# Kernel tuning notes

Measured on AMD Instinct MI355X. Metric: run time of the kernel, lower is better.

## Reference

```python
import jax, jax.numpy as jnp
import numpy as np

# ---- static config (mirrors init_kwargs + fixed setup box dims) ----
PC_MIN = jnp.array([0.0, -40.0, -3.0])
VOXEL_SIZE = jnp.array([0.05, 0.05, 0.1])
STRIDE = 4                     # pool_cfg.STRIDE and multi_scale_3d_strides['x_conv4']
EXTEND = 2.0                   # model_cfg.ROI_EXTEND_FACTOR
GRID_ZYX = (10, 400, 352)      # sparse spatial shape after stride-4 downsample [z,y,x]
# grid_size = round(extended_dims / voxel_size / STRIDE) for fixed dims [6.4,3.2,1.6]
GX, GY, GZ = 64, 32, 4
G = GX * GY * GZ
N_VOX, C = 200_000, 128
M = 64
KX, KY, KZ = 7, 7, 3


def setup_inputs() -> dict:
    key = jax.random.key(0)
    k1, k2, k3, k4, k5, k6, k7, k8, k9 = jax.random.split(key, 9)
    ctr = jnp.stack([
        jax.random.uniform(k1, (M,), minval=10.0, maxval=60.0),
        jax.random.uniform(k2, (M,), minval=-25.0, maxval=25.0),
        jax.random.uniform(k3, (M,), minval=-1.5, maxval=0.5)], axis=-1)
    dims = jnp.tile(jnp.array([[6.4, 3.2, 1.6]], jnp.float32), (M, 1))  # fixed -> static grid
    yaw = jax.random.uniform(k4, (M, 1), minval=-np.pi, maxval=np.pi)
    rois = jnp.concatenate([ctr, dims, yaw], axis=-1).astype(jnp.float32)
    proto_box = jnp.array([0.0, 0.0, 0.0, 6.4, 3.2, 1.6, 0.3], jnp.float32)
    voxel_feats = jax.random.normal(k5, (N_VOX, C), jnp.float32)
    feat_proto = jax.random.normal(k6, (1, KX, KY, KZ, C), jnp.float32) * 0.1
    zc = jax.random.randint(k7, (N_VOX,), 0, GRID_ZYX[0])
    yc = jax.random.randint(k8, (N_VOX,), 0, GRID_ZYX[1])
    xc = jax.random.randint(k9, (N_VOX,), 0, GRID_ZYX[2])
    voxel_coords = jnp.stack([jnp.zeros_like(zc), zc, yc, xc], -1).astype(jnp.int32)
    return dict(rois=rois, proto_box=proto_box, voxel_feats=voxel_feats,
                feat_proto=feat_proto, voxel_coords=voxel_coords)


def _dense_grid_points(box):
    # get_dense_grid_points: row-major (x,y,z) index order, matches torch nonzero()
    idx = jnp.stack(jnp.meshgrid(jnp.arange(GX), jnp.arange(GY), jnp.arange(GZ),
                                 indexing='ij'), -1).reshape(-1, 3).astype(jnp.float32)
    gs = jnp.array([GX, GY, GZ], jnp.float32)
    return (idx + 0.5) / gs * box[3:6] - box[3:6] / 2.0  # (G,3)


def _rotate_z(pts, ang):
    # common_utils.rotate_points_along_z: pts @ [[c,s,0],[-s,c,0],[0,0,1]]
    c, s = jnp.cos(ang), jnp.sin(ang)
    R = jnp.stack([jnp.stack([c, s, 0.0 * c]),
                   jnp.stack([-s, c, 0.0 * c]),
                   jnp.stack([0.0 * c, 0.0 * c, 1.0 + 0.0 * c])])
    return pts @ R


def reference(rois, proto_box, voxel_feats, feat_proto, voxel_coords):
    # generate_voxel2pinds: dense [Z,Y,X] grid of voxel row indices, -1 = empty
    v2p = -jnp.ones(GRID_ZYX, jnp.int32)
    v2p = v2p.at[voxel_coords[:, 1], voxel_coords[:, 2], voxel_coords[:, 3]].set(
        jnp.arange(N_VOX, dtype=jnp.int32))

    def per_roi(box):
        box = box.at[3:5].multiply(EXTEND)                 # xy_dim_extend
        local = _dense_grid_points(box)                    # (G,3)
        xyz = _rotate_z(local, box[6]) + box[:3]           # global roi grid points
        coords = jnp.floor((xyz - PC_MIN) / VOXEL_SIZE)    # '//' floor-div semantics
        coords = jnp.floor(coords / STRIDE).astype(jnp.int32)
        xc, yc, zc = coords[:, 0], coords[:, 1], coords[:, 2]
        inb = ((zc >= 0) & (zc < GRID_ZYX[0]) & (yc >= 0) & (yc < GRID_ZYX[1]) &
               (xc >= 0) & (xc < GRID_ZYX[2]))
        pidx = v2p[jnp.clip(zc, 0, GRID_ZYX[0] - 1),
                   jnp.clip(yc, 0, GRID_ZYX[1] - 1),
                   jnp.clip(xc, 0, GRID_ZYX[2] - 1)]
        valid = inb & (pidx >= 0)
        feat = jnp.where(valid[:, None], voxel_feats[jnp.clip(pidx, 0)], 0.0)  # (G,C)
        return feat, xyz

    feats, grid_xyz = jax.vmap(per_roi)(rois)              # (M,G,C), (M,G,3)
    vol = feats.reshape(M, GX, GY, GZ, C).transpose(0, 4, 1, 2, 3)   # NCDHW
    kern = feat_proto.transpose(0, 4, 1, 2, 3)                        # (1,C,KX,KY,KZ)
    pads = [(KX // 2,) * 2, (KY // 2,) * 2, (KZ // 2,) * 2]           # ceil((k-1)/2)
    mm = jax.lax.conv_general_dilated(vol, kern, (1, 1, 1), pads,
                                      dimension_numbers=('NCDHW', 'OIDHW', 'NCDHW'))
    # fresh BatchNorm3d(1) applied per-ROI (batch 1 each call): per-sample norm
    mu = jnp.mean(mm, axis=(1, 2, 3, 4), keepdims=True)
    var = jnp.var(mm, axis=(1, 2, 3, 4), keepdims=True)
    mm = (mm - mu) / jnp.sqrt(var + 1e-5)
    idx = jnp.minimum(jnp.argmax(mm.reshape(M, -1), axis=1), G - 1)
    sel = jnp.take_along_axis(grid_xyz, idx[:, None, None], axis=1)[:, 0, :]  # (M,3)
    rois_new = jnp.tile(proto_box[None], (M, 1))
    rois_new = rois_new.at[:, :3].set(sel)
    return rois_new
```

## Files before the change

kernel.cpp:

```cpp
#include <hip/hip_runtime.h>
#include <stdint.h>

#define GRID_Z 10
#define GRID_Y 400
#define GRID_X 352
#define NGRID (GRID_Z * GRID_Y * GRID_X)
#define NVOX 200000
#define CCH 128
#define MROI 64
#define GXD 64
#define GYD 32
#define GZD 4
#define GCELLS 8192
#define NTAPS 147
#define FPAD 132
#define TROWS 32

__device__ __forceinline__ void cell_xyz(const float* __restrict__ roi, int g,
                                         float& X, float& Y, float& Z) {
#pragma clang fp contract(off)
    int iz = g & 3;
    int iy = (g >> 2) & 31;
    int ix = g >> 7;
    float bx = roi[3] * 2.0f;
    float by = roi[4] * 2.0f;
    float bz = roi[5];
    float lx = (ix + 0.5f) / 64.0f * bx - bx / 2.0f;
    float ly = (iy + 0.5f) / 32.0f * by - by / 2.0f;
    float lz = (iz + 0.5f) / 4.0f  * bz - bz / 2.0f;
    float c = cosf(roi[6]);
    float s = sinf(roi[6]);
    X = lx * c + ly * (-s) + roi[0];
    Y = lx * s + ly * c    + roi[1];
    Z = lz + roi[2];
}

__device__ __forceinline__ int cell_to_pidx(const float* __restrict__ roi, int g,
                                            const int* __restrict__ v2p) {
#pragma clang fp contract(off)
    float X, Y, Z;
    cell_xyz(roi, g, X, Y, Z);
    float fx = floorf((X - 0.0f)     / 0.05f);
    float fy = floorf((Y - (-40.0f)) / 0.05f);
    float fz = floorf((Z - (-3.0f))  / 0.1f);
    int cx = (int)floorf(fx / 4.0f);
    int cy = (int)floorf(fy / 4.0f);
    int cz = (int)floorf(fz / 4.0f);
    int p = -1;
    if (cz >= 0 && cz < GRID_Z && cy >= 0 && cy < GRID_Y && cx >= 0 && cx < GRID_X)
        p = v2p[(cz * GRID_Y + cy) * GRID_X + cx];
    return p;
}

__global__ void k_scatter(const int* __restrict__ vcoords, int* __restrict__ v2p,
                          int* __restrict__ cnt) {
    int i = blockIdx.x * 256 + threadIdx.x;
    if (blockIdx.x == 0 && threadIdx.x < MROI) cnt[threadIdx.x] = 0;
    if (i >= NVOX) return;
    int z = vcoords[i * 4 + 1];
    int y = vcoords[i * 4 + 2];
    int x = vcoords[i * 4 + 3];
    atomicMax(&v2p[(z * GRID_Y + y) * GRID_X + x], i);
}

__global__ void k_build(const float* __restrict__ rois, const int* __restrict__ v2p,
                        unsigned* __restrict__ list, int* __restrict__ cnt) {
    int g = blockIdx.x * 256 + threadIdx.x;
    int m = blockIdx.y;
    int lane = threadIdx.x & 63;
    int p = cell_to_pidx(rois + m * 7, g, v2p);
    bool v = p >= 0;
    unsigned long long bal = __ballot(v);
    int nset = __popcll(bal);
    int base = 0;
    if (lane == 0 && nset) base = atomicAdd(&cnt[m], nset);
    base = __shfl(base, 0, 64);
    if (v) {
        int pos = __popcll(bal & ((1ull << lane) - 1ull));
        list[m * GCELLS + base + pos] = ((unsigned)p << 13) | (unsigned)g;
    }
}

__global__ __launch_bounds__(256) void k_dots(
        const float* __restrict__ vfeat, const float* __restrict__ fproto,
        const unsigned* __restrict__ list, const int* __restrict__ cnt,
        float* __restrict__ partial) {
    __shared__ float    sscore[GCELLS];
    __shared__ float    sfeat[TROWS * FPAD];
    __shared__ unsigned sg[TROWS];

    const int m    = blockIdx.y;
    const int NSd  = gridDim.x;
    const int tid  = threadIdx.x;
    const int w    = tid >> 6;
    const int lane = tid & 63;
    const int vi   = lane & 7;
    const int ti   = (lane >> 3) & 7;
    const int n    = cnt[m];
    const unsigned* lst = list + m * GCELLS;
    const int tbase = w * 40 + ti;

    int tkx[5], tky[5], tkz[5], tok[5];
    #pragma unroll
    for (int b = 0; b < 5; ++b) {
        int t = tbase + 8 * b;
        tok[b] = t < NTAPS;
        int tc = tok[b] ? t : (NTAPS - 1);
        int kx  = tc / 21;
        int rem = tc - kx * 21;
        tkx[b] = kx; tky[b] = rem / 3; tkz[b] = rem - tky[b] * 3;
    }
    {
        float4* s4 = (float4*)sscore;
        #pragma unroll
        for (int i = 0; i < GCELLS / 4 / 256; ++i)
            s4[tid + 256 * i] = make_float4(0.f, 0.f, 0.f, 0.f);
    }
    for (int vt0 = blockIdx.x * TROWS; vt0 < n; vt0 += TROWS * NSd) {
        __syncthreads();
        {
            int r = tid >> 3, q = tid & 7, v = vt0 + r;
            unsigned e = 0xFFFFFFFFu;
            if (v < n) e = lst[v];
            if (q == 0) sg[r] = e;
            if (e != 0xFFFFFFFFu) {
                int p = (int)(e >> 13);
                const float4* src = (const float4*)(vfeat + (size_t)p * CCH) + q * 4;
                float4* drow = (float4*)(sfeat + r * FPAD + q * 16);
                #pragma unroll
                for (int j = 0; j < 4; ++j) drow[j] = src[j];
            }
        }
        __syncthreads();
        float acc[4][5];
        #pragma unroll
        for (int a = 0; a < 4; ++a)
            #pragma unroll
            for (int b = 0; b < 5; ++b) acc[a][b] = 0.0f;
        #pragma unroll 1
        for (int k = 0; k < CCH; k += 4) {
            float4 f[4];
            #pragma unroll
            for (int a = 0; a < 4; ++a)
                f[a] = *(const float4*)&sfeat[(vi + 8 * a) * FPAD + k];
            float4 wv[5];
            #pragma unroll
            for (int b = 0; b < 5; ++b)
                wv[b] = *(const float4*)(fproto + (tbase + (tok[b] ? 8 * b : 0)) * CCH + k);
            #pragma unroll
            for (int a = 0; a < 4; ++a)
                #pragma unroll
                for (int b = 0; b < 5; ++b) {
                    acc[a][b] = fmaf(f[a].x, wv[b].x, acc[a][b]);
                    acc[a][b] = fmaf(f[a].y, wv[b].y, acc[a][b]);
                    acc[a][b] = fmaf(f[a].z, wv[b].z, acc[a][b]);
                    acc[a][b] = fmaf(f[a].w, wv[b].w, acc[a][b]);
                }
        }
        #pragma unroll
        for (int b = 0; b < 5; ++b) {
            if (!tok[b]) continue;
            #pragma unroll
            for (int a = 0; a < 4; ++a) {
                unsigned e = sg[vi + 8 * a];
                if (e == 0xFFFFFFFFu) continue;
                int g  = (int)(e & 8191u);
                int cx = (g >> 7)        - (tkx[b] - 3);
                int cy = ((g >> 2) & 31) - (tky[b] - 3);
                int cz = (g & 3)         - (tkz[b] - 1);
                if ((unsigned)cx < (unsigned)GXD && (unsigned)cy < (unsigned)GYD &&
                    (unsigned)cz < (unsigned)GZD)
                    atomicAdd(&sscore[(cx << 7) | (cy << 2) | cz], acc[a][b]);
            }
        }
    }
    __syncthreads();
    {
        float* dst = partial + ((size_t)m * NSd + blockIdx.x) * GCELLS;
        const float4* s4 = (const float4*)sscore;
        float4* d4 = (float4*)dst;
        #pragma unroll
        for (int i = 0; i < GCELLS / 4 / 256; ++i)
            d4[tid + 256 * i] = s4[tid + 256 * i];
    }
}

template <int NS>
__global__ __launch_bounds__(1024) void k_argfin(
        const float* __restrict__ partial, const float* __restrict__ rois,
        const float* __restrict__ pbox, float* __restrict__ out) {
    __shared__ unsigned long long red[1024];
    int m = blockIdx.x;
    int tid = threadIdx.x;
    const float* base = partial + (size_t)m * NS * GCELLS;
    unsigned long long bk = 0ull;
    #pragma unroll
    for (int i = 0; i < GCELLS / 1024; ++i) {
        int g = tid + 1024 * i;
        float v = 0.0f;
        #pragma unroll
        for (int s = 0; s < NS; ++s) v += base[s * GCELLS + g];
        unsigned ub  = __float_as_uint(v);
        unsigned key = (ub & 0x80000000u) ? ~ub : (ub | 0x80000000u);
        unsigned long long pk =
            ((unsigned long long)key << 32) | (unsigned)(GCELLS - 1 - g);
        bk = bk > pk ? bk : pk;
    }
    red[tid] = bk;
    __syncthreads();
    for (int s = 512; s > 0; s >>= 1) {
        if (tid < s) {
            unsigned long long o = red[tid + s];
            if (o > red[tid]) red[tid] = o;
        }
        __syncthreads();
    }
    if (tid == 0) {
        int g = (GCELLS - 1) - (int)(unsigned)(red[0] & 0xFFFFFFFFu);
        float X, Y, Z;
        cell_xyz(rois + m * 7, g, X, Y, Z);
        out[m * 7 + 0] = X;
        out[m * 7 + 1] = Y;
        out[m * 7 + 2] = Z;
        out[m * 7 + 3] = pbox[3];
        out[m * 7 + 4] = pbox[4];
        out[m * 7 + 5] = pbox[5];
        out[m * 7 + 6] = pbox[6];
    }
}

extern "C" void kernel_launch(void* const* d_in, const int* in_sizes, int n_in,
                              void* d_out, int out_size, void* d_ws, size_t ws_size,
                              hipStream_t stream) {
    const float* rois    = (const float*)d_in[0];
    const float* pbox    = (const float*)d_in[1];
    const float* vfeat   = (const float*)d_in[2];
    const float* fproto  = (const float*)d_in[3];
    const int*   vcoords = (const int*)d_in[4];
    float* out = (float*)d_out;

    int*      v2p  = (int*)d_ws;
    unsigned* list = (unsigned*)(v2p + NGRID);
    int*      cnt  = (int*)(list + MROI * GCELLS);
    size_t base = ((size_t)NGRID + (size_t)MROI * GCELLS) * 4 + 256;

    int NS; float* fpartial;
    if (ws_size >= base + (size_t)12 * MROI * GCELLS * 4) {
        NS = 12; fpartial = (float*)((char*)d_ws + base);
    } else if (ws_size >= base + (size_t)8 * MROI * GCELLS * 4) {
        NS = 8;  fpartial = (float*)((char*)d_ws + base);
    } else if (ws_size >= base + (size_t)4 * MROI * GCELLS * 4) {
        NS = 4;  fpartial = (float*)((char*)d_ws + base);
    } else {
        NS = 2;  fpartial = (float*)v2p;
    }

    hipMemsetAsync(v2p, 0xFF, (size_t)NGRID * 4, stream);
    k_scatter<<<(NVOX + 255) / 256, 256, 0, stream>>>(vcoords, v2p, cnt);
    k_build  <<<dim3(GCELLS / 256, MROI), 256, 0, stream>>>(rois, v2p, list, cnt);
    k_dots   <<<dim3(NS, MROI), 256, 0, stream>>>(vfeat, fproto, list, cnt, fpartial);
    if (NS == 12)      k_argfin<12><<<MROI, 1024, 0, stream>>>(fpartial, rois, pbox, out);
    else if (NS == 8)  k_argfin<8> <<<MROI, 1024, 0, stream>>>(fpartial, rois, pbox, out);
    else if (NS == 4)  k_argfin<4> <<<MROI, 1024, 0, stream>>>(fpartial, rois, pbox, out);
    else               k_argfin<2> <<<MROI, 1024, 0, stream>>>(fpartial, rois, pbox, out);
}
```

Measured before the change: 299.1 us.

## Enlarge dot tile, atomically reduce slice scores, distribute argmax with last-block finalize

```diff
diff --git a/kernel.cpp b/kernel.cpp
--- a/kernel.cpp
+++ b/kernel.cpp
@@ -14,7 +14,8 @@
 #define GCELLS 8192
 #define NTAPS 147
 #define FPAD 132
-#define TROWS 32
+#define TROWS 64
+#define NSLC 8
 
 __device__ __forceinline__ void cell_xyz(const float* __restrict__ roi, int g,
                                          float& X, float& Y, float& Z) {
@@ -52,10 +53,8 @@
     return p;
 }
 
-__global__ void k_scatter(const int* __restrict__ vcoords, int* __restrict__ v2p,
-                          int* __restrict__ cnt) {
+__global__ void k_scatter(const int* __restrict__ vcoords, int* __restrict__ v2p) {
     int i = blockIdx.x * 256 + threadIdx.x;
-    if (blockIdx.x == 0 && threadIdx.x < MROI) cnt[threadIdx.x] = 0;
     if (i >= NVOX) return;
     int z = vcoords[i * 4 + 1];
     int y = vcoords[i * 4 + 2];
@@ -84,7 +83,7 @@
 __global__ __launch_bounds__(256) void k_dots(
         const float* __restrict__ vfeat, const float* __restrict__ fproto,
         const unsigned* __restrict__ list, const int* __restrict__ cnt,
-        float* __restrict__ partial) {
+        float* __restrict__ score) {
     __shared__ float    sscore[GCELLS];
     __shared__ float    sfeat[TROWS * FPAD];
     __shared__ unsigned sg[TROWS];
@@ -119,36 +118,36 @@
     for (int vt0 = blockIdx.x * TROWS; vt0 < n; vt0 += TROWS * NSd) {
         __syncthreads();
         {
-            int r = tid >> 3, q = tid & 7, v = vt0 + r;
+            int r = tid >> 2, q = tid & 3, v = vt0 + r;
             unsigned e = 0xFFFFFFFFu;
             if (v < n) e = lst[v];
             if (q == 0) sg[r] = e;
             if (e != 0xFFFFFFFFu) {
                 int p = (int)(e >> 13);
-                const float4* src = (const float4*)(vfeat + (size_t)p * CCH) + q * 4;
-                float4* drow = (float4*)(sfeat + r * FPAD + q * 16);
+                const float4* src = (const float4*)(vfeat + (size_t)p * CCH) + q * 8;
+                float4* drow = (float4*)(sfeat + r * FPAD + q * 32);
                 #pragma unroll
-                for (int j = 0; j < 4; ++j) drow[j] = src[j];
+                for (int j = 0; j < 8; ++j) drow[j] = src[j];
             }
         }
         __syncthreads();
-        float acc[4][5];
-        #pragma unroll
-        for (int a = 0; a < 4; ++a)
+        float acc[8][5];
+        #pragma unroll
+        for (int a = 0; a < 8; ++a)
             #pragma unroll
             for (int b = 0; b < 5; ++b) acc[a][b] = 0.0f;
         #pragma unroll 1
         for (int k = 0; k < CCH; k += 4) {
-            float4 f[4];
-            #pragma unroll
-            for (int a = 0; a < 4; ++a)
+            float4 f[8];
+            #pragma unroll
+            for (int a = 0; a < 8; ++a)
                 f[a] = *(const float4*)&sfeat[(vi + 8 * a) * FPAD + k];
             float4 wv[5];
             #pragma unroll
             for (int b = 0; b < 5; ++b)
                 wv[b] = *(const float4*)(fproto + (tbase + (tok[b] ? 8 * b : 0)) * CCH + k);
             #pragma unroll
-            for (int a = 0; a < 4; ++a)
+            for (int a = 0; a < 8; ++a)
                 #pragma unroll
                 for (int b = 0; b < 5; ++b) {
                     acc[a][b] = fmaf(f[a].x, wv[b].x, acc[a][b]);
@@ -158,16 +157,17 @@
                 }
         }
         #pragma unroll
-        for (int b = 0; b < 5; ++b) {
-            if (!tok[b]) continue;
-            #pragma unroll
-            for (int a = 0; a < 4; ++a) {
-                unsigned e = sg[vi + 8 * a];
-                if (e == 0xFFFFFFFFu) continue;
-                int g  = (int)(e & 8191u);
-                int cx = (g >> 7)        - (tkx[b] - 3);
-                int cy = ((g >> 2) & 31) - (tky[b] - 3);
-                int cz = (g & 3)         - (tkz[b] - 1);
+        for (int a = 0; a < 8; ++a) {
+            unsigned e = sg[vi + 8 * a];
+            if (e == 0xFFFFFFFFu) continue;
+            int g  = (int)(e & 8191u);
+            int gx = g >> 7, gy = (g >> 2) & 31, gz = g & 3;
+            #pragma unroll
+            for (int b = 0; b < 5; ++b) {
+                if (!tok[b]) continue;
+                int cx = gx - (tkx[b] - 3);
+                int cy = gy - (tky[b] - 3);
+                int cz = gz - (tkz[b] - 1);
                 if ((unsigned)cx < (unsigned)GXD && (unsigned)cy < (unsigned)GYD &&
                     (unsigned)cz < (unsigned)GZD)
                     atomicAdd(&sscore[(cx << 7) | (cy << 2) | cz], acc[a][b]);
@@ -175,57 +175,66 @@
         }
     }
     __syncthreads();
-    {
-        float* dst = partial + ((size_t)m * NSd + blockIdx.x) * GCELLS;
-        const float4* s4 = (const float4*)sscore;
-        float4* d4 = (float4*)dst;
-        #pragma unroll
-        for (int i = 0; i < GCELLS / 4 / 256; ++i)
-            d4[tid + 256 * i] = s4[tid + 256 * i];
-    }
-}
-
-template <int NS>
-__global__ __launch_bounds__(1024) void k_argfin(
-        const float* __restrict__ partial, const float* __restrict__ rois,
-        const float* __restrict__ pbox, float* __restrict__ out) {
-    __shared__ unsigned long long red[1024];
-    int m = blockIdx.x;
-    int tid = threadIdx.x;
-    const float* base = partial + (size_t)m * NS * GCELLS;
+    if (blockIdx.x * TROWS < n) {
+        float* dst = score + (size_t)m * GCELLS;
+        #pragma unroll
+        for (int i = 0; i < GCELLS / 256; ++i) {
+            float v = sscore[tid + 256 * i];
+            if (__float_as_uint(v) != 0u)
+                atomicAdd(&dst[tid + 256 * i], v);
+        }
+    }
+}
+
+__global__ __launch_bounds__(256) void k_amax(
+        const float* __restrict__ score, const float* __restrict__ rois,
+        const float* __restrict__ pbox, unsigned long long* __restrict__ best,
+        unsigned* __restrict__ done, float* __restrict__ out) {
+    __shared__ unsigned long long red[256];
+    __shared__ unsigned lastflag;
+    const int tid = threadIdx.x;
+    const int m = blockIdx.y;
+    const float* base = score + (size_t)m * GCELLS;
+    int c0 = blockIdx.x * (GCELLS / 8);
     unsigned long long bk = 0ull;
     #pragma unroll
-    for (int i = 0; i < GCELLS / 1024; ++i) {
-        int g = tid + 1024 * i;
-        float v = 0.0f;
-        #pragma unroll
-        for (int s = 0; s < NS; ++s) v += base[s * GCELLS + g];
+    for (int i = 0; i < GCELLS / 8 / 256; ++i) {
+        int c = c0 + tid + 256 * i;
+        float v = base[c];
         unsigned ub  = __float_as_uint(v);
         unsigned key = (ub & 0x80000000u) ? ~ub : (ub | 0x80000000u);
         unsigned long long pk =
-            ((unsigned long long)key << 32) | (unsigned)(GCELLS - 1 - g);
+            ((unsigned long long)key << 32) | (unsigned)(GCELLS - 1 - c);
         bk = bk > pk ? bk : pk;
     }
     red[tid] = bk;
     __syncthreads();
-    for (int s = 512; s > 0; s >>= 1) {
-        if (tid < s) {
-            unsigned long long o = red[tid + s];
+    for (int st = 128; st > 0; st >>= 1) {
+        if (tid < st) {
+            unsigned long long o = red[tid + st];
             if (o > red[tid]) red[tid] = o;
         }
         __syncthreads();
     }
     if (tid == 0) {
-        int g = (GCELLS - 1) - (int)(unsigned)(red[0] & 0xFFFFFFFFu);
+        atomicMax(&best[m], red[0]);
+        __threadfence();
+        unsigned d = atomicAdd(done, 1u);
+        lastflag = (d == gridDim.x * gridDim.y - 1u);
+    }
+    __syncthreads();
+    if (lastflag && tid < MROI) {
+        unsigned long long bv = atomicMax(&best[tid], 0ull);
+        int g = (GCELLS - 1) - (int)(unsigned)(bv & 0xFFFFFFFFu);
         float X, Y, Z;
-        cell_xyz(rois + m * 7, g, X, Y, Z);
-        out[m * 7 + 0] = X;
-        out[m * 7 + 1] = Y;
-        out[m * 7 + 2] = Z;
-        out[m * 7 + 3] = pbox[3];
-        out[m * 7 + 4] = pbox[4];
-        out[m * 7 + 5] = pbox[5];
-        out[m * 7 + 6] = pbox[6];
+        cell_xyz(rois + tid * 7, g, X, Y, Z);
+        out[tid * 7 + 0] = X;
+        out[tid * 7 + 1] = Y;
+        out[tid * 7 + 2] = Z;
+        out[tid * 7 + 3] = pbox[3];
+        out[tid * 7 + 4] = pbox[4];
+        out[tid * 7 + 5] = pbox[5];
+        out[tid * 7 + 6] = pbox[6];
     }
 }
 
@@ -241,26 +250,16 @@
 
     int*      v2p  = (int*)d_ws;
     unsigned* list = (unsigned*)(v2p + NGRID);
-    int*      cnt  = (int*)(list + MROI * GCELLS);
-    size_t base = ((size_t)NGRID + (size_t)MROI * GCELLS) * 4 + 256;
-
-    int NS; float* fpartial;
-    if (ws_size >= base + (size_t)12 * MROI * GCELLS * 4) {
-        NS = 12; fpartial = (float*)((char*)d_ws + base);
-    } else if (ws_size >= base + (size_t)8 * MROI * GCELLS * 4) {
-        NS = 8;  fpartial = (float*)((char*)d_ws + base);
-    } else if (ws_size >= base + (size_t)4 * MROI * GCELLS * 4) {
-        NS = 4;  fpartial = (float*)((char*)d_ws + base);
-    } else {
-        NS = 2;  fpartial = (float*)v2p;
-    }
+    float*    score = (float*)(list + (size_t)MROI * GCELLS);
+    unsigned long long* best = (unsigned long long*)(score + (size_t)MROI * GCELLS);
+    int*      cnt  = (int*)(best + MROI);
+    unsigned* done = (unsigned*)(cnt + MROI);
+    size_t zbytes = (size_t)((char*)(done + 1) - (char*)score);
 
     hipMemsetAsync(v2p, 0xFF, (size_t)NGRID * 4, stream);
-    k_scatter<<<(NVOX + 255) / 256, 256, 0, stream>>>(vcoords, v2p, cnt);
+    hipMemsetAsync(score, 0, zbytes, stream);
+    k_scatter<<<(NVOX + 255) / 256, 256, 0, stream>>>(vcoords, v2p);
     k_build  <<<dim3(GCELLS / 256, MROI), 256, 0, stream>>>(rois, v2p, list, cnt);
-    k_dots   <<<dim3(NS, MROI), 256, 0, stream>>>(vfeat, fproto, list, cnt, fpartial);
-    if (NS == 12)      k_argfin<12><<<MROI, 1024, 0, stream>>>(fpartial, rois, pbox, out);
-    else if (NS == 8)  k_argfin<8> <<<MROI, 1024, 0, stream>>>(fpartial, rois, pbox, out);
-    else if (NS == 4)  k_argfin<4> <<<MROI, 1024, 0, stream>>>(fpartial, rois, pbox, out);
-    else               k_argfin<2> <<<MROI, 1024, 0, stream>>>(fpartial, rois, pbox, out);
-}
+    k_dots   <<<dim3(NSLC, MROI), 256, 0, stream>>>(vfeat, fproto, list, cnt, score);
+    k_amax   <<<dim3(8, MROI), 256, 0, stream>>>(score, rois, pbox, best, done, out);
+}
```

New measurement: 343.3 us. 14.8% more time.

## Fuse argmax finalize into dots kernel via atomic score accumulation and last-block reduction

Applied to the files above, without the earlier changes.

```diff
diff --git a/kernel.cpp b/kernel.cpp
--- a/kernel.cpp
+++ b/kernel.cpp
@@ -15,6 +15,7 @@
 #define NTAPS 147
 #define FPAD 132
 #define TROWS 32
+#define NSLC 12
 
 __device__ __forceinline__ void cell_xyz(const float* __restrict__ roi, int g,
                                          float& X, float& Y, float& Z) {
@@ -53,9 +54,12 @@
 }
 
 __global__ void k_scatter(const int* __restrict__ vcoords, int* __restrict__ v2p,
-                          int* __restrict__ cnt) {
+                          int* __restrict__ cnt, unsigned* __restrict__ rdone) {
     int i = blockIdx.x * 256 + threadIdx.x;
-    if (blockIdx.x == 0 && threadIdx.x < MROI) cnt[threadIdx.x] = 0;
+    if (blockIdx.x == 0 && threadIdx.x < MROI) {
+        cnt[threadIdx.x] = 0;
+        rdone[threadIdx.x] = 0u;
+    }
     if (i >= NVOX) return;
     int z = vcoords[i * 4 + 1];
     int y = vcoords[i * 4 + 2];
@@ -64,9 +68,11 @@
 }
 
 __global__ void k_build(const float* __restrict__ rois, const int* __restrict__ v2p,
-                        unsigned* __restrict__ list, int* __restrict__ cnt) {
+                        unsigned* __restrict__ list, int* __restrict__ cnt,
+                        float* __restrict__ score) {
     int g = blockIdx.x * 256 + threadIdx.x;
     int m = blockIdx.y;
+    score[(size_t)m * GCELLS + g] = 0.0f;
     int lane = threadIdx.x & 63;
     int p = cell_to_pidx(rois + m * 7, g, v2p);
     bool v = p >= 0;
@@ -84,10 +90,13 @@
 __global__ __launch_bounds__(256) void k_dots(
         const float* __restrict__ vfeat, const float* __restrict__ fproto,
         const unsigned* __restrict__ list, const int* __restrict__ cnt,
-        float* __restrict__ partial) {
+        float* __restrict__ score, unsigned* __restrict__ rdone,
+        const float* __restrict__ rois, const float* __restrict__ pbox,
+        float* __restrict__ out) {
     __shared__ float    sscore[GCELLS];
     __shared__ float    sfeat[TROWS * FPAD];
     __shared__ unsigned sg[TROWS];
+    __shared__ unsigned lastflag;
 
     const int m    = blockIdx.y;
     const int NSd  = gridDim.x;
@@ -116,6 +125,7 @@
         for (int i = 0; i < GCELLS / 4 / 256; ++i)
             s4[tid + 256 * i] = make_float4(0.f, 0.f, 0.f, 0.f);
     }
+    const bool contrib = (blockIdx.x * TROWS < n);
     for (int vt0 = blockIdx.x * TROWS; vt0 < n; vt0 += TROWS * NSd) {
         __syncthreads();
         {
@@ -158,16 +168,17 @@
                 }
         }
         #pragma unroll
-        for (int b = 0; b < 5; ++b) {
-            if (!tok[b]) continue;
-            #pragma unroll
-            for (int a = 0; a < 4; ++a) {
-                unsigned e = sg[vi + 8 * a];
-                if (e == 0xFFFFFFFFu) continue;
-                int g  = (int)(e & 8191u);
-                int cx = (g >> 7)        - (tkx[b] - 3);
-                int cy = ((g >> 2) & 31) - (tky[b] - 3);
-                int cz = (g & 3)         - (tkz[b] - 1);
+        for (int a = 0; a < 4; ++a) {
+            unsigned e = sg[vi + 8 * a];
+            if (e == 0xFFFFFFFFu) continue;
+            int g  = (int)(e & 8191u);
+            int gx = g >> 7, gy = (g >> 2) & 31, gz = g & 3;
+            #pragma unroll
+            for (int b = 0; b < 5; ++b) {
+                if (!tok[b]) continue;
+                int cx = gx - (tkx[b] - 3);
+                int cy = gy - (tky[b] - 3);
+                int cz = gz - (tkz[b] - 1);
                 if ((unsigned)cx < (unsigned)GXD && (unsigned)cy < (unsigned)GYD &&
                     (unsigned)cz < (unsigned)GZD)
                     atomicAdd(&sscore[(cx << 7) | (cy << 2) | cz], acc[a][b]);
@@ -175,42 +186,40 @@
         }
     }
     __syncthreads();
-    {
-        float* dst = partial + ((size_t)m * NSd + blockIdx.x) * GCELLS;
-        const float4* s4 = (const float4*)sscore;
-        float4* d4 = (float4*)dst;
-        #pragma unroll
-        for (int i = 0; i < GCELLS / 4 / 256; ++i)
-            d4[tid + 256 * i] = s4[tid + 256 * i];
-    }
-}
-
-template <int NS>
-__global__ __launch_bounds__(1024) void k_argfin(
-        const float* __restrict__ partial, const float* __restrict__ rois,
-        const float* __restrict__ pbox, float* __restrict__ out) {
-    __shared__ unsigned long long red[1024];
-    int m = blockIdx.x;
-    int tid = threadIdx.x;
-    const float* base = partial + (size_t)m * NS * GCELLS;
+    float* dst = score + (size_t)m * GCELLS;
+    if (contrib) {
+        #pragma unroll
+        for (int i = 0; i < GCELLS / 256; ++i) {
+            float v = sscore[tid + 256 * i];
+            if (__float_as_uint(v) != 0u)
+                atomicAdd(&dst[tid + 256 * i], v);
+        }
+    }
+    __threadfence();
+    if (tid == 0) {
+        unsigned d = atomicAdd(&rdone[m], 1u);
+        lastflag = (d == (unsigned)NSd - 1u);
+    }
+    __syncthreads();
+    if (!lastflag) return;
+
     unsigned long long bk = 0ull;
     #pragma unroll
-    for (int i = 0; i < GCELLS / 1024; ++i) {
-        int g = tid + 1024 * i;
-        float v = 0.0f;
-        #pragma unroll
-        for (int s = 0; s < NS; ++s) v += base[s * GCELLS + g];
+    for (int i = 0; i < GCELLS / 256; ++i) {
+        int c = tid + 256 * i;
+        float v = atomicAdd(&dst[c], 0.0f);
         unsigned ub  = __float_as_uint(v);
         unsigned key = (ub & 0x80000000u) ? ~ub : (ub | 0x80000000u);
         unsigned long long pk =
-            ((unsigned long long)key << 32) | (unsigned)(GCELLS - 1 - g);
+            ((unsigned long long)key << 32) | (unsigned)(GCELLS - 1 - c);
         bk = bk > pk ? bk : pk;
     }
+    unsigned long long* red = reinterpret_cast<unsigned long long*>(sscore);
     red[tid] = bk;
     __syncthreads();
-    for (int s = 512; s > 0; s >>= 1) {
-        if (tid < s) {
-            unsigned long long o = red[tid + s];
+    for (int st = 128; st > 0; st >>= 1) {
+        if (tid < st) {
+            unsigned long long o = red[tid + st];
             if (o > red[tid]) red[tid] = o;
         }
         __syncthreads();
@@ -239,28 +248,15 @@
     const int*   vcoords = (const int*)d_in[4];
     float* out = (float*)d_out;
 
-    int*      v2p  = (int*)d_ws;
-    unsigned* list = (unsigned*)(v2p + NGRID);
-    int*      cnt  = (int*)(list + MROI * GCELLS);
-    size_t base = ((size_t)NGRID + (size_t)MROI * GCELLS) * 4 + 256;
-
-    int NS; float* fpartial;
-    if (ws_size >= base + (size_t)12 * MROI * GCELLS * 4) {
-        NS = 12; fpartial = (float*)((char*)d_ws + base);
-    } else if (ws_size >= base + (size_t)8 * MROI * GCELLS * 4) {
-        NS = 8;  fpartial = (float*)((char*)d_ws + base);
-    } else if (ws_size >= base + (size_t)4 * MROI * GCELLS * 4) {
-        NS = 4;  fpartial = (float*)((char*)d_ws + base);
-    } else {
-        NS = 2;  fpartial = (float*)v2p;
-    }
+    int*      v2p   = (int*)d_ws;
+    unsigned* list  = (unsigned*)(v2p + NGRID);
+    float*    score = (float*)(list + (size_t)MROI * GCELLS);
+    int*      cnt   = (int*)(score + (size_t)MROI * GCELLS);
+    unsigned* rdone = (unsigned*)(cnt + MROI);
 
     hipMemsetAsync(v2p, 0xFF, (size_t)NGRID * 4, stream);
-    k_scatter<<<(NVOX + 255) / 256, 256, 0, stream>>>(vcoords, v2p, cnt);
-    k_build  <<<dim3(GCELLS / 256, MROI), 256, 0, stream>>>(rois, v2p, list, cnt);
-    k_dots   <<<dim3(NS, MROI), 256, 0, stream>>>(vfeat, fproto, list, cnt, fpartial);
-    if (NS == 12)      k_argfin<12><<<MROI, 1024, 0, stream>>>(fpartial, rois, pbox, out);
-    else if (NS == 8)  k_argfin<8> <<<MROI, 1024, 0, stream>>>(fpartial, rois, pbox, out);
-    else if (NS == 4)  k_argfin<4> <<<MROI, 1024, 0, stream>>>(fpartial, rois, pbox, out);
-    else               k_argfin<2> <<<MROI, 1024, 0, stream>>>(fpartial, rois, pbox, out);
-}
+    k_scatter<<<(NVOX + 255) / 256, 256, 0, stream>>>(vcoords, v2p, cnt, rdone);
+    k_build  <<<dim3(GCELLS / 256, MROI), 256, 0, stream>>>(rois, v2p, list, cnt, score);
+    k_dots   <<<dim3(NSLC, MROI), 256, 0, stream>>>(vfeat, fproto, list, cnt, score,
+                                                    rdone, rois, pbox, out);
+}
```

Result: slower. 347.4 us (+16.2%).

## Compute voxel-tap dot products with split-bf16 MFMA instead of scalar FMA

Applied to the files above, without the earlier changes.

```diff
diff --git a/kernel.cpp b/kernel.cpp
--- a/kernel.cpp
+++ b/kernel.cpp
@@ -13,8 +13,22 @@
 #define GZD 4
 #define GCELLS 8192
 #define NTAPS 147
-#define FPAD 132
 #define TROWS 32
+#define NSLC 12
+#define PITCH 136
+#define NTT 10
+#define BFRAGN (NTT * 4 * 64)
+
+typedef short bf16x8 __attribute__((ext_vector_type(8)));
+typedef float f32x4 __attribute__((ext_vector_type(4)));
+
+__device__ __forceinline__ unsigned f2bf(float x) {
+    unsigned u = __float_as_uint(x);
+    return (u + 0x7FFFu + ((u >> 16) & 1u)) >> 16;
+}
+__device__ __forceinline__ float bf2f(unsigned h) {
+    return __uint_as_float(h << 16);
+}
 
 __device__ __forceinline__ void cell_xyz(const float* __restrict__ roi, int g,
                                          float& X, float& Y, float& Z) {
@@ -52,6 +66,32 @@
     return p;
 }
 
+__global__ void k_prep(const float* __restrict__ fproto,
+                       uint4* __restrict__ bH, uint4* __restrict__ bL) {
+    int tT   = blockIdx.x;
+    int ks   = threadIdx.x >> 6;
+    int lane = threadIdx.x & 63;
+    int tap  = tT * 16 + (lane & 15);
+    int k0   = ks * 32 + (lane >> 4) * 8;
+    unsigned hi[8], lo[8];
+    #pragma unroll
+    for (int j = 0; j < 8; ++j) {
+        float x = (tap < NTAPS) ? fproto[tap * CCH + k0 + j] : 0.0f;
+        unsigned h = f2bf(x);
+        float r = x - bf2f(h);
+        hi[j] = h;
+        lo[j] = f2bf(r);
+    }
+    uint4 uh, ul;
+    uh.x = hi[0] | (hi[1] << 16); uh.y = hi[2] | (hi[3] << 16);
+    uh.z = hi[4] | (hi[5] << 16); uh.w = hi[6] | (hi[7] << 16);
+    ul.x = lo[0] | (lo[1] << 16); ul.y = lo[2] | (lo[3] << 16);
+    ul.z = lo[4] | (lo[5] << 16); ul.w = lo[6] | (lo[7] << 16);
+    int idx = (tT * 4 + ks) * 64 + lane;
+    bH[idx] = uh;
+    bL[idx] = ul;
+}
+
 __global__ void k_scatter(const int* __restrict__ vcoords, int* __restrict__ v2p,
                           int* __restrict__ cnt) {
     int i = blockIdx.x * 256 + threadIdx.x;
@@ -82,33 +122,34 @@
 }
 
 __global__ __launch_bounds__(256) void k_dots(
-        const float* __restrict__ vfeat, const float* __restrict__ fproto,
-        const unsigned* __restrict__ list, const int* __restrict__ cnt,
-        float* __restrict__ partial) {
-    __shared__ float    sscore[GCELLS];
-    __shared__ float    sfeat[TROWS * FPAD];
+        const float* __restrict__ vfeat, const uint4* __restrict__ bH,
+        const uint4* __restrict__ bL, const unsigned* __restrict__ list,
+        const int* __restrict__ cnt, float* __restrict__ partial) {
+    __shared__ float sscore[GCELLS];
+    __shared__ __align__(16) unsigned short sAh[TROWS * PITCH];
+    __shared__ __align__(16) unsigned short sAl[TROWS * PITCH];
     __shared__ unsigned sg[TROWS];
 
     const int m    = blockIdx.y;
-    const int NSd  = gridDim.x;
     const int tid  = threadIdx.x;
     const int w    = tid >> 6;
     const int lane = tid & 63;
-    const int vi   = lane & 7;
-    const int ti   = (lane >> 3) & 7;
+    const int rt   = w >> 1;
+    const int th   = w & 1;
+    const int col  = lane & 15;
+    const int kg   = lane >> 4;
     const int n    = cnt[m];
     const unsigned* lst = list + m * GCELLS;
-    const int tbase = w * 40 + ti;
 
     int tkx[5], tky[5], tkz[5], tok[5];
     #pragma unroll
-    for (int b = 0; b < 5; ++b) {
-        int t = tbase + 8 * b;
-        tok[b] = t < NTAPS;
-        int tc = tok[b] ? t : (NTAPS - 1);
+    for (int tt = 0; tt < 5; ++tt) {
+        int t = th * 80 + tt * 16 + col;
+        tok[tt] = t < NTAPS;
+        int tc = tok[tt] ? t : 0;
         int kx  = tc / 21;
         int rem = tc - kx * 21;
-        tkx[b] = kx; tky[b] = rem / 3; tkz[b] = rem - tky[b] * 3;
+        tkx[tt] = kx; tky[tt] = rem / 3; tkz[tt] = rem - tky[tt] * 3;
     }
     {
         float4* s4 = (float4*)sscore;
@@ -116,7 +157,7 @@
         for (int i = 0; i < GCELLS / 4 / 256; ++i)
             s4[tid + 256 * i] = make_float4(0.f, 0.f, 0.f, 0.f);
     }
-    for (int vt0 = blockIdx.x * TROWS; vt0 < n; vt0 += TROWS * NSd) {
+    for (int vt0 = blockIdx.x * TROWS; vt0 < n; vt0 += TROWS * NSLC) {
         __syncthreads();
         {
             int r = tid >> 3, q = tid & 7, v = vt0 + r;
@@ -126,57 +167,79 @@
             if (e != 0xFFFFFFFFu) {
                 int p = (int)(e >> 13);
                 const float4* src = (const float4*)(vfeat + (size_t)p * CCH) + q * 4;
-                float4* drow = (float4*)(sfeat + r * FPAD + q * 16);
+                unsigned hb[16], lb[16];
                 #pragma unroll
-                for (int j = 0; j < 4; ++j) drow[j] = src[j];
+                for (int j = 0; j < 4; ++j) {
+                    float4 s = src[j];
+                    float xs[4] = {s.x, s.y, s.z, s.w};
+                    #pragma unroll
+                    for (int c = 0; c < 4; ++c) {
+                        unsigned h = f2bf(xs[c]);
+                        hb[j * 4 + c] = h;
+                        lb[j * 4 + c] = f2bf(xs[c] - bf2f(h));
+                    }
+                }
+                uint4 h0, h1, l0, l1;
+                h0.x = hb[0]  | (hb[1]  << 16); h0.y = hb[2]  | (hb[3]  << 16);
+                h0.z = hb[4]  | (hb[5]  << 16); h0.w = hb[6]  | (hb[7]  << 16);
+                h1.x = hb[8]  | (hb[9]  << 16); h1.y = hb[10] | (hb[11] << 16);
+                h1.z = hb[12] | (hb[13] << 16); h1.w = hb[14] | (hb[15] << 16);
+                l0.x = lb[0]  | (lb[1]  << 16); l0.y = lb[2]  | (lb[3]  << 16);
+                l0.z = lb[4]  | (lb[5]  << 16); l0.w = lb[6]  | (lb[7]  << 16);
+                l1.x = lb[8]  | (lb[9]  << 16); l1.y = lb[10] | (lb[11] << 16);
+                l1.z = lb[12] | (lb[13] << 16); l1.w = lb[14] | (lb[15] << 16);
+                uint4* dh = (uint4*)((char*)sAh + r * (PITCH * 2) + q * 32);
+                uint4* dl = (uint4*)((char*)sAl + r * (PITCH * 2) + q * 32);
+                dh[0] = h0; dh[1] = h1;
+                dl[0] = l0; dl[1] = l1;
             }
         }
         __syncthreads();
-        float acc[4][5];
-        #pragma unroll
-        for (int a = 0; a < 4; ++a)
+        bf16x8 ah[4], al[4];
+        const char* abh = (const char*)sAh + (rt * 16 + col) * (PITCH * 2);
+        const char* abl = (const char*)sAl + (rt * 16 + col) * (PITCH * 2);
+        #pragma unroll
+        for (int ks = 0; ks < 4; ++ks) {
+            ah[ks] = *(const bf16x8*)(abh + ks * 64 + kg * 16);
+            al[ks] = *(const bf16x8*)(abl + ks * 64 + kg * 16);
+        }
+        f32x4 acc[5];
+        #pragma unroll
+        for (int tt = 0; tt < 5; ++tt) acc[tt] = (f32x4){0.f, 0.f, 0.f, 0.f};
+        #pragma unroll
+        for (int tt = 0; tt < 5; ++tt) {
+            const int bi = ((th * 5 + tt) * 4) * 64 + lane;
             #pragma unroll
-            for (int b = 0; b < 5; ++b) acc[a][b] = 0.0f;
-        #pragma unroll 1
-        for (int k = 0; k < CCH; k += 4) {
-            float4 f[4];
+            for (int ks = 0; ks < 4; ++ks) {
+                uint4 uh = bH[bi + ks * 64];
+                uint4 ul = bL[bi + ks * 64];
+                bf16x8 bh = *(bf16x8*)&uh;
+                bf16x8 bl = *(bf16x8*)&ul;
+                acc[tt] = __builtin_amdgcn_mfma_f32_16x16x32_bf16(ah[ks], bh, acc[tt], 0, 0, 0);
+                acc[tt] = __builtin_amdgcn_mfma_f32_16x16x32_bf16(ah[ks], bl, acc[tt], 0, 0, 0);
+                acc[tt] = __builtin_amdgcn_mfma_f32_16x16x32_bf16(al[ks], bh, acc[tt], 0, 0, 0);
+            }
+        }
+        #pragma unroll
+        for (int tt = 0; tt < 5; ++tt) {
+            if (!tok[tt]) continue;
             #pragma unroll
-            for (int a = 0; a < 4; ++a)
-                f[a] = *(const float4*)&sfeat[(vi + 8 * a) * FPAD + k];
-            float4 wv[5];
-            #pragma unroll
-            for (int b = 0; b < 5; ++b)
-                wv[b] = *(const float4*)(fproto + (tbase + (tok[b] ? 8 * b : 0)) * CCH + k);
-            #pragma unroll
-            for (int a = 0; a < 4; ++a)
-                #pragma unroll
-                for (int b = 0; b < 5; ++b) {
-                    acc[a][b] = fmaf(f[a].x, wv[b].x, acc[a][b]);
-                    acc[a][b] = fmaf(f[a].y, wv[b].y, acc[a][b]);
-                    acc[a][b] = fmaf(f[a].z, wv[b].z, acc[a][b]);
-                    acc[a][b] = fmaf(f[a].w, wv[b].w, acc[a][b]);
-                }
-        }
-        #pragma unroll
-        for (int b = 0; b < 5; ++b) {
-            if (!tok[b]) continue;
-            #pragma unroll
-            for (int a = 0; a < 4; ++a) {
-                unsigned e = sg[vi + 8 * a];
+            for (int rg = 0; rg < 4; ++rg) {
+                unsigned e = sg[rt * 16 + kg * 4 + rg];
                 if (e == 0xFFFFFFFFu) continue;
                 int g  = (int)(e & 8191u);
-                int cx = (g >> 7)        - (tkx[b] - 3);
-                int cy = ((g >> 2) & 31) - (tky[b] - 3);
-                int cz = (g & 3)         - (tkz[b] - 1);
+                int cx = (g >> 7)        - (tkx[tt] - 3);
+                int cy = ((g >> 2) & 31) - (tky[tt] - 3);
+                int cz = (g & 3)         - (tkz[tt] - 1);
                 if ((unsigned)cx < (unsigned)GXD && (unsigned)cy < (unsigned)GYD &&
                     (unsigned)cz < (unsigned)GZD)
-                    atomicAdd(&sscore[(cx << 7) | (cy << 2) | cz], acc[a][b]);
+                    atomicAdd(&sscore[(cx << 7) | (cy << 2) | cz], acc[tt][rg]);
             }
         }
     }
     __syncthreads();
     {
-        float* dst = partial + ((size_t)m * NSd + blockIdx.x) * GCELLS;
+        float* dst = partial + ((size_t)m * NSLC + blockIdx.x) * GCELLS;
         const float4* s4 = (const float4*)sscore;
         float4* d4 = (float4*)dst;
         #pragma unroll
@@ -185,21 +248,20 @@
     }
 }
 
-template <int NS>
 __global__ __launch_bounds__(1024) void k_argfin(
         const float* __restrict__ partial, const float* __restrict__ rois,
         const float* __restrict__ pbox, float* __restrict__ out) {
     __shared__ unsigned long long red[1024];
     int m = blockIdx.x;
     int tid = threadIdx.x;
-    const float* base = partial + (size_t)m * NS * GCELLS;
+    const float* base = partial + (size_t)m * NSLC * GCELLS;
     unsigned long long bk = 0ull;
     #pragma unroll
     for (int i = 0; i < GCELLS / 1024; ++i) {
         int g = tid + 1024 * i;
         float v = 0.0f;
         #pragma unroll
-        for (int s = 0; s < NS; ++s) v += base[s * GCELLS + g];
+        for (int s = 0; s < NSLC; ++s) v += base[s * GCELLS + g];
         unsigned ub  = __float_as_uint(v);
         unsigned key = (ub & 0x80000000u) ? ~ub : (ub | 0x80000000u);
         unsigned long long pk =
@@ -239,28 +301,17 @@
     const int*   vcoords = (const int*)d_in[4];
     float* out = (float*)d_out;
 
-    int*      v2p  = (int*)d_ws;
-    unsigned* list = (unsigned*)(v2p + NGRID);
-    int*      cnt  = (int*)(list + MROI * GCELLS);
-    size_t base = ((size_t)NGRID + (size_t)MROI * GCELLS) * 4 + 256;
-
-    int NS; float* fpartial;
-    if (ws_size >= base + (size_t)12 * MROI * GCELLS * 4) {
-        NS = 12; fpartial = (float*)((char*)d_ws + base);
-    } else if (ws_size >= base + (size_t)8 * MROI * GCELLS * 4) {
-        NS = 8;  fpartial = (float*)((char*)d_ws + base);
-    } else if (ws_size >= base + (size_t)4 * MROI * GCELLS * 4) {
-        NS = 4;  fpartial = (float*)((char*)d_ws + base);
-    } else {
-        NS = 2;  fpartial = (float*)v2p;
-    }
+    int*      v2p     = (int*)d_ws;
+    unsigned* list    = (unsigned*)(v2p + NGRID);
+    float*    partial = (float*)(list + (size_t)MROI * GCELLS);
+    uint4*    bH      = (uint4*)(partial + (size_t)NSLC * MROI * GCELLS);
+    uint4*    bL      = bH + BFRAGN;
+    int*      cnt     = (int*)(bL + BFRAGN);
 
     hipMemsetAsync(v2p, 0xFF, (size_t)NGRID * 4, stream);
+    k_prep   <<<NTT, 256, 0, stream>>>(fproto, bH, bL);
     k_scatter<<<(NVOX + 255) / 256, 256, 0, stream>>>(vcoords, v2p, cnt);
     k_build  <<<dim3(GCELLS / 256, MROI), 256, 0, stream>>>(rois, v2p, list, cnt);
-    k_dots   <<<dim3(NS, MROI), 256, 0, stream>>>(vfeat, fproto, list, cnt, fpartial);
-    if (NS == 12)      k_argfin<12><<<MROI, 1024, 0, stream>>>(fpartial, rois, pbox, out);
-    else if (NS == 8)  k_argfin<8> <<<MROI, 1024, 0, stream>>>(fpartial, rois, pbox, out);
-    else if (NS == 4)  k_argfin<4> <<<MROI, 1024, 0, stream>>>(fpartial, rois, pbox, out);
-    else               k_argfin<2> <<<MROI, 1024, 0, stream>>>(fpartial, rois, pbox, out);
-}
+    k_dots   <<<dim3(NSLC, MROI), 256, 0, stream>>>(vfeat, bH, bL, list, cnt, partial);
+    k_argfin <<<MROI, 1024, 0, stream>>>(partial, rois, pbox, out);
+}
```

Result: faster. 281.7 us (-5.8%).
